# Kernel tuning notes

Measured on AMD Instinct MI355X. Metric: run time of the kernel, lower is better.

## Reference

```python
import jax, jax.numpy as jnp
import numpy as np
from jax import lax

EPS = 1e-5  # torch LayerNorm default

def setup_inputs() -> dict:
    key = jax.random.key(0)
    ks = jax.random.split(key, 8)
    B, T = 512, 4096
    x = jax.random.normal(ks[0], (B, T, 16), dtype=jnp.float32)
    # shared causal conv: Conv1d(in=8, out=16, k=3) -> weight (O,I,K), bias (O,)
    conv_w = jax.random.normal(ks[1], (16, 8, 3), dtype=jnp.float32) * 0.2
    conv_b = jax.random.normal(ks[2], (16,), dtype=jnp.float32) * 0.05
    # dominance MLP: Linear(32,16) -> ReLU -> Linear(16,2); stored (in,out)
    w1 = jax.random.normal(ks[3], (32, 16), dtype=jnp.float32) * 0.17
    b1 = jax.random.normal(ks[4], (16,), dtype=jnp.float32) * 0.05
    w2 = jax.random.normal(ks[5], (16, 2), dtype=jnp.float32) * 0.25
    b2 = jax.random.normal(ks[6], (2,), dtype=jnp.float32) * 0.05
    ln_g = jnp.ones((16,), dtype=jnp.float32)
    ln_b = jnp.zeros((16,), dtype=jnp.float32)
    return {"x": x, "conv_w": conv_w, "conv_b": conv_b, "w1": w1, "b1": b1,
            "w2": w2, "b2": b2, "ln_g": ln_g, "ln_b": ln_b}

def reference(x, conv_w, conv_b, w1, b1, w2, b2, ln_g, ln_b):
    B = x.shape[0]
    X_L = x[:, :, :8]   # (B,T,8)
    X_R = x[:, :, 8:]   # (B,T,8)
    # shared conv applied to both arms: stack along batch for one conv call
    stacked = jnp.concatenate([X_L, X_R], axis=0).transpose(0, 2, 1)  # (2B,8,T)
    h = lax.conv_general_dilated(stacked, conv_w, window_strides=(1,),
                                 padding=[(2, 0)],  # causal left-pad for k=3
                                 dimension_numbers=("NCH", "OIH", "NCH"))
    h = jax.nn.relu(h + conv_b[None, :, None]).transpose(0, 2, 1)  # (2B,T,16)
    H_L, H_R = h[:B], h[B:]
    H_cat = jnp.concatenate([H_L, H_R], axis=-1)  # (B,T,32)
    hidden = jax.nn.relu(jnp.einsum("btf,fh->bth", H_cat, w1) + b1)
    alpha_logits = jnp.einsum("bth,hc->btc", hidden, w2) + b2  # (B,T,2)
    alphas = jax.nn.softmax(alpha_logits, axis=-1)
    tilde_X = jnp.concatenate([alphas[:, :, 0:1] * X_L,
                               alphas[:, :, 1:2] * X_R], axis=-1)
    y = x + tilde_X
    mu = jnp.mean(y, axis=-1, keepdims=True)
    var = jnp.mean(jnp.square(y - mu), axis=-1, keepdims=True)
    out_X = (y - mu) * jax.lax.rsqrt(var + EPS) * ln_g + ln_b
    return (out_X, alphas)
```

## Files before the change

kernel.cpp:

```cpp
#include <hip/hip_runtime.h>

#define BB 512
#define TT 4096
#define EPSF 1e-5f

__device__ __forceinline__ void load_row(const float* __restrict__ p, float* dst) {
    const float4* q = reinterpret_cast<const float4*>(p);
#pragma unroll
    for (int i = 0; i < 4; ++i) {
        float4 v = q[i];
        dst[4 * i + 0] = v.x; dst[4 * i + 1] = v.y;
        dst[4 * i + 2] = v.z; dst[4 * i + 3] = v.w;
    }
}

__global__ __launch_bounds__(256) void bimanual_fused_kernel(
    const float* __restrict__ x,
    const float* __restrict__ conv_w,
    const float* __restrict__ conv_b,
    const float* __restrict__ w1,
    const float* __restrict__ b1,
    const float* __restrict__ w2,
    const float* __restrict__ b2,
    const float* __restrict__ ln_g,
    const float* __restrict__ ln_b,
    float* __restrict__ out)
{
    const int pos = blockIdx.x * blockDim.x + threadIdx.x;
    const int t = pos & (TT - 1);
    const size_t rowbase = (size_t)pos * 16;

    float xw[3][16];
    load_row(x + rowbase, xw[2]);
    if (t >= 1) {
        load_row(x + rowbase - 16, xw[1]);
    } else {
#pragma unroll
        for (int i = 0; i < 16; ++i) xw[1][i] = 0.f;
    }
    if (t >= 2) {
        load_row(x + rowbase - 32, xw[0]);
    } else {
#pragma unroll
        for (int i = 0; i < 16; ++i) xw[0][i] = 0.f;
    }

    float h[32];
#pragma unroll
    for (int o = 0; o < 16; ++o) {
        float aL = conv_b[o];
        float aR = aL;
#pragma unroll
        for (int i = 0; i < 8; ++i) {
#pragma unroll
            for (int k = 0; k < 3; ++k) {
                const float w = conv_w[(o * 8 + i) * 3 + k];
                aL = fmaf(xw[k][i], w, aL);
                aR = fmaf(xw[k][8 + i], w, aR);
            }
        }
        h[o]      = fmaxf(aL, 0.f);
        h[16 + o] = fmaxf(aR, 0.f);
    }

    float hid[16];
#pragma unroll
    for (int j = 0; j < 16; ++j) {
        float a = b1[j];
#pragma unroll
        for (int f = 0; f < 32; ++f) {
            a = fmaf(h[f], w1[f * 16 + j], a);
        }
        hid[j] = fmaxf(a, 0.f);
    }

    float l0 = b2[0], l1 = b2[1];
#pragma unroll
    for (int j = 0; j < 16; ++j) {
        l0 = fmaf(hid[j], w2[j * 2 + 0], l0);
        l1 = fmaf(hid[j], w2[j * 2 + 1], l1);
    }

    const float m  = fmaxf(l0, l1);
    const float e0 = __expf(l0 - m);
    const float e1 = __expf(l1 - m);
    const float inv = 1.f / (e0 + e1);
    const float a0 = e0 * inv;
    const float a1 = e1 * inv;

    float y[16];
    const float g0 = 1.f + a0;
    const float g1 = 1.f + a1;
#pragma unroll
    for (int i = 0; i < 8; ++i)  y[i]     = xw[2][i]     * g0;
#pragma unroll
    for (int i = 0; i < 8; ++i)  y[8 + i] = xw[2][8 + i] * g1;

    float s = 0.f;
#pragma unroll
    for (int i = 0; i < 16; ++i) s += y[i];
    const float mu = s * (1.f / 16.f);
    float v = 0.f;
#pragma unroll
    for (int i = 0; i < 16; ++i) {
        const float d = y[i] - mu;
        v = fmaf(d, d, v);
    }
    const float rs = rsqrtf(v * (1.f / 16.f) + EPSF);

    float o16[16];
#pragma unroll
    for (int i = 0; i < 16; ++i) {
        o16[i] = fmaf((y[i] - mu) * rs, ln_g[i], ln_b[i]);
    }

    float4* od = reinterpret_cast<float4*>(out + rowbase);
#pragma unroll
    for (int i = 0; i < 4; ++i) {
        od[i] = make_float4(o16[4 * i + 0], o16[4 * i + 1],
                            o16[4 * i + 2], o16[4 * i + 3]);
    }
    float2* oa = reinterpret_cast<float2*>(out + (size_t)BB * TT * 16 + (size_t)pos * 2);
    *oa = make_float2(a0, a1);
}

extern "C" void kernel_launch(void* const* d_in, const int* in_sizes, int n_in,
                              void* d_out, int out_size, void* d_ws, size_t ws_size,
                              hipStream_t stream) {
    const float* x      = (const float*)d_in[0];
    const float* conv_w = (const float*)d_in[1];
    const float* conv_b = (const float*)d_in[2];
    const float* w1     = (const float*)d_in[3];
    const float* b1     = (const float*)d_in[4];
    const float* w2     = (const float*)d_in[5];
    const float* b2     = (const float*)d_in[6];
    const float* ln_g   = (const float*)d_in[7];
    const float* ln_b   = (const float*)d_in[8];
    float* out = (float*)d_out;

    const int total = BB * TT;
    dim3 block(256);
    dim3 grid(total / 256);
    hipLaunchKernelGGL(bimanual_fused_kernel, grid, block, 0, stream,
                       x, conv_w, conv_b, w1, b1, w2, b2, ln_g, ln_b, out);
}
```

Baseline: 290.6 us.

## Compute conv and first MLP layer with bf16 MFMA via LDS staging

Replaces the per-thread scalar FP32 conv and 32x16 linear layer with bf16 16x16x32 MFMA instructions. Input rows plus a two-row causal halo are converted to bf16 and staged in shared memory, so the three overlapping input loads per thread become shared reuse. Intermediate activations pass between the stages through LDS, with block barriers between them. This cuts ALU work and redundant global loads, but lowers the precision of the conv and hidden activations to bf16 and adds shared-memory traffic and synchronisation.

```diff
diff --git a/kernel.cpp b/kernel.cpp
--- a/kernel.cpp
+++ b/kernel.cpp
@@ -4,17 +4,21 @@
 #define TT 4096
 #define EPSF 1e-5f
 
-__device__ __forceinline__ void load_row(const float* __restrict__ p, float* dst) {
-    const float4* q = reinterpret_cast<const float4*>(p);
-#pragma unroll
-    for (int i = 0; i < 4; ++i) {
-        float4 v = q[i];
-        dst[4 * i + 0] = v.x; dst[4 * i + 1] = v.y;
-        dst[4 * i + 2] = v.z; dst[4 * i + 3] = v.w;
-    }
+typedef __attribute__((ext_vector_type(8))) short bf16x8;
+typedef __attribute__((ext_vector_type(4))) float f32x4;
+
+__device__ __forceinline__ unsigned short f2b(float f) {
+    union { float f; unsigned u; } v; v.f = f;
+    unsigned r = (v.u + 0x7fffu + ((v.u >> 16) & 1u)) >> 16;
+    return (unsigned short)r;
 }
 
-__global__ __launch_bounds__(256) void bimanual_fused_kernel(
+#define XROWB   48
+#define HROWB   80
+#define HIDROWB 80
+#define H_OFF   20480
+
+__global__ __launch_bounds__(256) void bimanual_mfma_kernel(
     const float* __restrict__ x,
     const float* __restrict__ conv_w,
     const float* __restrict__ conv_b,
@@ -26,102 +30,144 @@
     const float* __restrict__ ln_b,
     float* __restrict__ out)
 {
-    const int pos = blockIdx.x * blockDim.x + threadIdx.x;
-    const int t = pos & (TT - 1);
-    const size_t rowbase = (size_t)pos * 16;
+    __shared__ __align__(16) unsigned char lds[40960];
 
-    float xw[3][16];
-    load_row(x + rowbase, xw[2]);
-    if (t >= 1) {
-        load_row(x + rowbase - 16, xw[1]);
-    } else {
+    const int tid  = threadIdx.x;
+    const int lane = tid & 63;
+    const int w    = tid >> 6;
+    const int col  = lane & 15;
+    const int g    = lane >> 4;
+    const int p0   = blockIdx.x << 8;
+
+    bf16x8 Bc, B1;
 #pragma unroll
-        for (int i = 0; i < 16; ++i) xw[1][i] = 0.f;
+    for (int j = 0; j < 8; ++j) {
+        float wc = (g < 3) ? conv_w[(col * 8 + j) * 3 + g] : 0.f;
+        Bc[j] = (short)f2b(wc);
+        B1[j] = (short)f2b(w1[(g * 8 + j) * 16 + col]);
     }
-    if (t >= 2) {
-        load_row(x + rowbase - 32, xw[0]);
-    } else {
+    const float bias_c = conv_b[col];
+    const float bias_1 = b1[col];
+
+    const bool tz = ((blockIdx.x & 15) == 0);
+    for (int r = tid; r < 258; r += 256) {
+        unsigned u[8];
+        if (tz && r < 2) {
 #pragma unroll
-        for (int i = 0; i < 16; ++i) xw[0][i] = 0.f;
+            for (int k = 0; k < 8; ++k) u[k] = 0u;
+        } else {
+            const float4* src = reinterpret_cast<const float4*>(x + (size_t)(p0 + r - 2) * 16);
+            float f[16];
+#pragma unroll
+            for (int k = 0; k < 4; ++k) {
+                float4 v = src[k];
+                f[4 * k] = v.x; f[4 * k + 1] = v.y; f[4 * k + 2] = v.z; f[4 * k + 3] = v.w;
+            }
+#pragma unroll
+            for (int k = 0; k < 8; ++k)
+                u[k] = (unsigned)f2b(f[2 * k]) | ((unsigned)f2b(f[2 * k + 1]) << 16);
+        }
+        *reinterpret_cast<uint4*>(lds + r * XROWB)      = make_uint4(u[0], u[1], u[2], u[3]);
+        *reinterpret_cast<uint4*>(lds + r * XROWB + 16) = make_uint4(u[4], u[5], u[6], u[7]);
     }
+    __syncthreads();
 
-    float h[32];
+    const bf16x8 zfrag = {0, 0, 0, 0, 0, 0, 0, 0};
 #pragma unroll
-    for (int o = 0; o < 16; ++o) {
-        float aL = conv_b[o];
-        float aR = aL;
+    for (int m = 0; m < 4; ++m) {
+        const int posm = (w << 6) + (m << 4);
+        const int arow = posm + col + ((g < 3) ? g : 0);
+        bf16x8 AL = *reinterpret_cast<const bf16x8*>(lds + arow * XROWB);
+        bf16x8 AR = *reinterpret_cast<const bf16x8*>(lds + arow * XROWB + 16);
+        if (g == 3) { AL = zfrag; AR = zfrag; }
+        f32x4 accL = {bias_c, bias_c, bias_c, bias_c};
+        f32x4 accR = accL;
+        accL = __builtin_amdgcn_mfma_f32_16x16x32_bf16(AL, Bc, accL, 0, 0, 0);
+        accR = __builtin_amdgcn_mfma_f32_16x16x32_bf16(AR, Bc, accR, 0, 0, 0);
+        const int prow = posm + (g << 2);
 #pragma unroll
-        for (int i = 0; i < 8; ++i) {
+        for (int q = 0; q < 4; ++q) {
+            *reinterpret_cast<unsigned short*>(lds + H_OFF + (prow + q) * HROWB + col * 2)
+                = f2b(fmaxf(accL[q], 0.f));
+            *reinterpret_cast<unsigned short*>(lds + H_OFF + (prow + q) * HROWB + 32 + col * 2)
+                = f2b(fmaxf(accR[q], 0.f));
+        }
+    }
+    __syncthreads();
+
 #pragma unroll
-            for (int k = 0; k < 3; ++k) {
-                const float w = conv_w[(o * 8 + i) * 3 + k];
-                aL = fmaf(xw[k][i], w, aL);
-                aR = fmaf(xw[k][8 + i], w, aR);
-            }
-        }
-        h[o]      = fmaxf(aL, 0.f);
-        h[16 + o] = fmaxf(aR, 0.f);
+    for (int m = 0; m < 4; ++m) {
+        const int posm = (w << 6) + (m << 4);
+        bf16x8 A = *reinterpret_cast<const bf16x8*>(
+            lds + H_OFF + (posm + col) * HROWB + g * 16);
+        f32x4 acc = {bias_1, bias_1, bias_1, bias_1};
+        acc = __builtin_amdgcn_mfma_f32_16x16x32_bf16(A, B1, acc, 0, 0, 0);
+        const int prow = posm + (g << 2);
+#pragma unroll
+        for (int q = 0; q < 4; ++q)
+            *reinterpret_cast<float*>(lds + (prow + q) * HIDROWB + col * 4) = fmaxf(acc[q], 0.f);
     }
+    __syncthreads();
 
     float hid[16];
+    const float4* hp = reinterpret_cast<const float4*>(lds + tid * HIDROWB);
 #pragma unroll
-    for (int j = 0; j < 16; ++j) {
-        float a = b1[j];
-#pragma unroll
-        for (int f = 0; f < 32; ++f) {
-            a = fmaf(h[f], w1[f * 16 + j], a);
-        }
-        hid[j] = fmaxf(a, 0.f);
+    for (int k = 0; k < 4; ++k) {
+        float4 v = hp[k];
+        hid[4 * k] = v.x; hid[4 * k + 1] = v.y; hid[4 * k + 2] = v.z; hid[4 * k + 3] = v.w;
     }
-
     float l0 = b2[0], l1 = b2[1];
 #pragma unroll
     for (int j = 0; j < 16; ++j) {
-        l0 = fmaf(hid[j], w2[j * 2 + 0], l0);
-        l1 = fmaf(hid[j], w2[j * 2 + 1], l1);
+        l0 = fmaf(hid[j], w2[2 * j], l0);
+        l1 = fmaf(hid[j], w2[2 * j + 1], l1);
     }
-
-    const float m  = fmaxf(l0, l1);
-    const float e0 = __expf(l0 - m);
-    const float e1 = __expf(l1 - m);
+    const float mm = fmaxf(l0, l1);
+    const float e0 = __expf(l0 - mm);
+    const float e1 = __expf(l1 - mm);
     const float inv = 1.f / (e0 + e1);
     const float a0 = e0 * inv;
     const float a1 = e1 * inv;
 
+    const size_t rowbase = (size_t)(p0 + tid) * 16;
+    float xv[16];
+    const float4* xp = reinterpret_cast<const float4*>(x + rowbase);
+#pragma unroll
+    for (int k = 0; k < 4; ++k) {
+        float4 v = xp[k];
+        xv[4 * k] = v.x; xv[4 * k + 1] = v.y; xv[4 * k + 2] = v.z; xv[4 * k + 3] = v.w;
+    }
     float y[16];
     const float g0 = 1.f + a0;
     const float g1 = 1.f + a1;
 #pragma unroll
-    for (int i = 0; i < 8; ++i)  y[i]     = xw[2][i]     * g0;
+    for (int i = 0; i < 8; ++i) y[i] = xv[i] * g0;
 #pragma unroll
-    for (int i = 0; i < 8; ++i)  y[8 + i] = xw[2][8 + i] * g1;
+    for (int i = 0; i < 8; ++i) y[8 + i] = xv[8 + i] * g1;
 
     float s = 0.f;
 #pragma unroll
     for (int i = 0; i < 16; ++i) s += y[i];
     const float mu = s * (1.f / 16.f);
-    float v = 0.f;
+    float var = 0.f;
 #pragma unroll
     for (int i = 0; i < 16; ++i) {
         const float d = y[i] - mu;
-        v = fmaf(d, d, v);
+        var = fmaf(d, d, var);
     }
-    const float rs = rsqrtf(v * (1.f / 16.f) + EPSF);
-
-    float o16[16];
-#pragma unroll
-    for (int i = 0; i < 16; ++i) {
-        o16[i] = fmaf((y[i] - mu) * rs, ln_g[i], ln_b[i]);
-    }
+    const float rs = rsqrtf(var * (1.f / 16.f) + EPSF);
 
     float4* od = reinterpret_cast<float4*>(out + rowbase);
 #pragma unroll
-    for (int i = 0; i < 4; ++i) {
-        od[i] = make_float4(o16[4 * i + 0], o16[4 * i + 1],
-                            o16[4 * i + 2], o16[4 * i + 3]);
+    for (int k = 0; k < 4; ++k) {
+        float o0 = fmaf((y[4 * k]     - mu) * rs, ln_g[4 * k],     ln_b[4 * k]);
+        float o1 = fmaf((y[4 * k + 1] - mu) * rs, ln_g[4 * k + 1], ln_b[4 * k + 1]);
+        float o2 = fmaf((y[4 * k + 2] - mu) * rs, ln_g[4 * k + 2], ln_b[4 * k + 2]);
+        float o3 = fmaf((y[4 * k + 3] - mu) * rs, ln_g[4 * k + 3], ln_b[4 * k + 3]);
+        od[k] = make_float4(o0, o1, o2, o3);
     }
-    float2* oa = reinterpret_cast<float2*>(out + (size_t)BB * TT * 16 + (size_t)pos * 2);
-    *oa = make_float2(a0, a1);
+    *reinterpret_cast<float2*>(out + (size_t)BB * TT * 16 + (size_t)(p0 + tid) * 2)
+        = make_float2(a0, a1);
 }
 
 extern "C" void kernel_launch(void* const* d_in, const int* in_sizes, int n_in,
@@ -141,6 +187,6 @@
     const int total = BB * TT;
     dim3 block(256);
     dim3 grid(total / 256);
-    hipLaunchKernelGGL(bimanual_fused_kernel, grid, block, 0, stream,
+    hipLaunchKernelGGL(bimanual_mfma_kernel, grid, block, 0, stream,
                        x, conv_w, conv_b, w1, b1, w2, b2, ln_g, ln_b, out);
 }
```

Result: faster. 275.4 us (-5.2%).
